# Optimization experiments

Hardware: AMD Instinct MI355X
Metric: run time of the kernel (lower is better)

The kernel has to match this reference:

```python
import jax, jax.numpy as jnp
import numpy as np


def _conv1x1(x, w):
    # x [N,I,D,H,W], w [O,I]
    return jnp.einsum('nidhw,oi->nodhw', x, w)


def _conv3x3(x, w):
    return jax.lax.conv_general_dilated(
        x, w, window_strides=(1, 1, 1), padding=[(1, 1)] * 3,
        dimension_numbers=('NCDHW', 'OIDHW', 'NCDHW'))


def _interp_axis(x, out_len, axis):
    # linear interpolation along one axis, align_corners=True
    in_len = x.shape[axis]
    scale = (in_len - 1) / (out_len - 1)
    pos = jnp.arange(out_len, dtype=x.dtype) * scale
    lo = jnp.clip(jnp.floor(pos).astype(jnp.int32), 0, in_len - 1)
    hi = jnp.minimum(lo + 1, in_len - 1)
    frac = pos - lo.astype(x.dtype)
    shp = [1] * x.ndim
    shp[axis] = out_len
    frac = frac.reshape(shp)
    return jnp.take(x, lo, axis=axis) * (1 - frac) + jnp.take(x, hi, axis=axis) * frac


def _upsample_trilinear_ac(x, size):
    for ax, s in zip((2, 3, 4), size):
        x = _interp_axis(x, s, ax)
    return x


def _grid_sample_3d(inp, grid):
    # inp [N,C,D,H,W]; grid [N,Do,Ho,Wo,3] with channels (x=w, y=h, z=d) in [-1,1]
    # matches torch grid_sample defaults: trilinear, align_corners=False, zeros padding
    N, C, D, H, W = inp.shape
    ix = ((grid[..., 0] + 1) * W - 1) * 0.5
    iy = ((grid[..., 1] + 1) * H - 1) * 0.5
    iz = ((grid[..., 2] + 1) * D - 1) * 0.5
    x0 = jnp.floor(ix).astype(jnp.int32)
    y0 = jnp.floor(iy).astype(jnp.int32)
    z0 = jnp.floor(iz).astype(jnp.int32)
    fx = ix - x0.astype(inp.dtype)
    fy = iy - y0.astype(inp.dtype)
    fz = iz - z0.astype(inp.dtype)
    flat = inp.reshape(N, C, D * H * W)
    out = jnp.zeros((N, C) + grid.shape[1:4], dtype=inp.dtype)
    for dz, wz in ((0, 1 - fz), (1, fz)):
        for dy, wy in ((0, 1 - fy), (1, fy)):
            for dx, wx in ((0, 1 - fx), (1, fx)):
                zc = z0 + dz
                yc = y0 + dy
                xc = x0 + dx
                valid = (zc >= 0) & (zc < D) & (yc >= 0) & (yc < H) & (xc >= 0) & (xc < W)
                idx = (jnp.clip(zc, 0, D - 1) * H + jnp.clip(yc, 0, H - 1)) * W + jnp.clip(xc, 0, W - 1)
                vals = jax.vmap(lambda f, i: f[:, i])(flat, idx)  # [N,C,Do,Ho,Wo]
                w = (wz * wy * wx) * valid.astype(inp.dtype)
                out = out + vals * w[:, None]
    return out


def _point_reinforce(x, w_atten, w_conv):
    # SE-style: global avg pool -> 1x1 conv -> sigmoid -> residual scale -> 1x1 conv
    pooled = jnp.mean(x, axis=(2, 3, 4), keepdims=True)
    atten = jax.nn.sigmoid(_conv1x1(pooled, w_atten))
    x = x + x * atten
    return _conv1x1(x, w_conv)


def _forward(x, y, w_down_h, w_down_l, w_flow, w_att_atten, w_att_conv):
    D, H, W = x.shape[2:]
    low = _conv1x1(x, w_down_l)
    low = _point_reinforce(low, w_att_atten, w_att_conv)
    hf = _conv1x1(y, w_down_h)
    hf = _upsample_trilinear_ac(hf, (D, H, W))
    flow = _conv3x3(jnp.concatenate([hf, low], axis=1), w_flow)  # [N,3,D,H,W]
    # coordinate grid, channel order (w, h, d) as in the original flow_warp
    gw = jnp.broadcast_to(jnp.arange(W, dtype=x.dtype)[None, None, :], (D, H, W))
    gh = jnp.broadcast_to(jnp.arange(H, dtype=x.dtype)[None, :, None], (D, H, W))
    gd = jnp.broadcast_to(jnp.arange(D, dtype=x.dtype)[:, None, None], (D, H, W))
    grid = jnp.stack([gw, gh, gd], axis=0)[None]  # [1,3,D,H,W]
    norm = jnp.array([W, H, D], dtype=x.dtype)
    # NOTE: faithful to original -- divides by size only (grid ends up in [0,1), not [-1,1])
    vgrid = jnp.transpose(grid + flow, (0, 2, 3, 4, 1)) / norm  # [N,D,H,W,3]
    return _grid_sample_3d(y, vgrid)


def setup_inputs() -> dict:
    key = jax.random.key(0)
    ks = jax.random.split(key, 7)
    inplane_l, inplane_h, outplane = 64, 128, 64
    x = jax.random.normal(ks[0], (2, inplane_l, 16, 64, 64), dtype=jnp.float32)
    y = jax.random.normal(ks[1], (2, inplane_h, 8, 32, 32), dtype=jnp.float32)
    s = 0.05
    w_down_h = jax.random.normal(ks[2], (outplane, inplane_h), dtype=jnp.float32) * s
    w_down_l = jax.random.normal(ks[3], (outplane, inplane_l), dtype=jnp.float32) * s
    w_flow = jax.random.normal(ks[4], (3, 2 * outplane, 3, 3, 3), dtype=jnp.float32) * s
    w_att_atten = jax.random.normal(ks[5], (inplane_l, inplane_l), dtype=jnp.float32) * s
    w_att_conv = jax.random.normal(ks[6], (inplane_l, inplane_l), dtype=jnp.float32) * s
    return {'x': x, 'y': y, 'w_down_h': w_down_h, 'w_down_l': w_down_l,
            'w_flow': w_flow, 'w_att_atten': w_att_atten, 'w_att_conv': w_att_conv}


def reference(x, y, w_down_h, w_down_l, w_flow, w_att_atten, w_att_conv):
    return _forward(x, y, w_down_h, w_down_l, w_flow, w_att_atten, w_att_conv)
```

## Files before the change

kernel.cpp:

```cpp
#include <hip/hip_runtime.h>
#include <math.h>


#define MEANX_OFF  0
#define WCOMBT_OFF 128
#define HF_OFF     8320
#define LOW2_OFF   1056896
#define HFUP_OFF   9445504
#define VG_OFF     17834112
#define ZPAGE_OFF  18227328

__global__ __launch_bounds__(256) void kearly(const float* __restrict__ x,
                                              const float* __restrict__ y,
                                              const float* __restrict__ wdh,
                                              float* __restrict__ meanx,
                                              float* __restrict__ hf,
                                              float* __restrict__ zpage) {
    const int blk = blockIdx.x;
    if (blk < 128) {
        if (blk == 0 && threadIdx.x < 64) zpage[threadIdx.x] = 0.f;
        int ch = blk;
        const float4* base = (const float4*)(x + (size_t)ch * 65536);
        float s = 0.f;
        for (int j = threadIdx.x; j < 16384; j += 256) {
            float4 v = base[j];
            s += v.x + v.y + v.z + v.w;
        }
        __shared__ float red[256];
        red[threadIdx.x] = s;
        __syncthreads();
        for (int off = 128; off > 0; off >>= 1) {
            if (threadIdx.x < off) red[threadIdx.x] += red[threadIdx.x + off];
            __syncthreads();
        }
        if (threadIdx.x == 0) meanx[ch] = red[0] * (1.0f / 65536.0f);
    } else {
        const int b = blk - 128;
        const int n = b >> 7;
        const int r = b & 127;
        const int os = r & 3;
        const int tile = r >> 2;
        const int p = tile * 256 + threadIdx.x;
        const float* yb = y + (size_t)n * 128 * 8192 + p;

        float acc[16];
#pragma unroll
        for (int o = 0; o < 16; ++o) acc[o] = 0.f;

        for (int i = 0; i < 128; i += 4) {
            const float yi0 = yb[(size_t)(i + 0) * 8192];
            const float yi1 = yb[(size_t)(i + 1) * 8192];
            const float yi2 = yb[(size_t)(i + 2) * 8192];
            const float yi3 = yb[(size_t)(i + 3) * 8192];
#pragma unroll
            for (int o = 0; o < 16; ++o) {
                float a = acc[o];
                a = fmaf(wdh[(os * 16 + o) * 128 + i + 0], yi0, a);
                a = fmaf(wdh[(os * 16 + o) * 128 + i + 1], yi1, a);
                a = fmaf(wdh[(os * 16 + o) * 128 + i + 2], yi2, a);
                a = fmaf(wdh[(os * 16 + o) * 128 + i + 3], yi3, a);
                acc[o] = a;
            }
        }
        float* ob = hf + (size_t)(n * 64 + os * 16) * 8192 + p;
#pragma unroll
        for (int o = 0; o < 16; ++o)
            ob[(size_t)o * 8192] = acc[o];
    }
}

__global__ __launch_bounds__(256) void kprep(const float* __restrict__ wdl,
                                             const float* __restrict__ watt,
                                             const float* __restrict__ wconv,
                                             const float* __restrict__ meanx,
                                             float* __restrict__ wcombT) {
    const int n = blockIdx.x;
    const int tid = threadIdx.x;
    __shared__ float s_wdl[4096];
    __shared__ float s_wcT[4096];
    __shared__ float pooled[64], sc[64];
    for (int k = tid; k < 4096; k += 256) {
        s_wdl[k] = wdl[k];
        int o = k >> 6, j = k & 63;
        s_wcT[j * 64 + o] = wconv[k];
    }
    __syncthreads();
    if (tid < 64) {
        float p = 0.f;
        for (int i = 0; i < 64; ++i) p += s_wdl[tid * 64 + i] * meanx[n * 64 + i];
        pooled[tid] = p;
    }
    __syncthreads();
    if (tid < 64) {
        float a = 0.f;
        for (int i = 0; i < 64; ++i) a += watt[tid * 64 + i] * pooled[i];
        sc[tid] = 1.f + 1.f / (1.f + expf(-a));
    }
    __syncthreads();
    for (int k = 0; k < 16; ++k) {
        const int idx = tid + 256 * k;
        const int o = idx & 63, i = idx >> 6;
        float acc = 0.f;
#pragma unroll 8
        for (int j = 0; j < 64; ++j)
            acc += s_wcT[j * 64 + o] * (sc[j] * s_wdl[j * 64 + i]);
        wcombT[n * 4096 + i * 64 + o] = acc;
    }
}

__global__ __launch_bounds__(256) void kmid(const float* __restrict__ x,
                                            const float* __restrict__ wcombT,
                                            const float* __restrict__ hf,
                                            float* __restrict__ low2,
                                            float* __restrict__ hfup) {
    const int blk = blockIdx.x;
    if (blk < 512) {
        const int b = blk;
        const int n = b >> 8;
        const int r = b & 255;
        const int os = r & 1;
        const int tile = r >> 1;
        const int p = tile * 512 + 2 * threadIdx.x;
        const float* xb = x + (size_t)n * 64 * 65536 + p;
        const float* wr = wcombT + n * 4096 + os * 32;

        float2 acc[32];
#pragma unroll
        for (int o = 0; o < 32; ++o) acc[o] = make_float2(0.f, 0.f);

        for (int i = 0; i < 64; i += 2) {
            const float2 xi0 = *(const float2*)(xb + (size_t)(i + 0) * 65536);
            const float2 xi1 = *(const float2*)(xb + (size_t)(i + 1) * 65536);
#pragma unroll
            for (int o = 0; o < 32; ++o) {
                const float w0 = wr[(i + 0) * 64 + o];
                const float w1 = wr[(i + 1) * 64 + o];
                acc[o].x = fmaf(w0, xi0.x, acc[o].x);
                acc[o].y = fmaf(w0, xi0.y, acc[o].y);
                acc[o].x = fmaf(w1, xi1.x, acc[o].x);
                acc[o].y = fmaf(w1, xi1.y, acc[o].y);
            }
        }
        float* ob = low2 + (size_t)(n * 64 + os * 32) * 65536 + p;
#pragma unroll
        for (int o = 0; o < 32; ++o)
            *(float2*)(ob + (size_t)o * 65536) = acc[o];
    } else {
        int id2 = (blk - 512) * 256 + threadIdx.x;
        int wp = id2 & 31, h = (id2 >> 5) & 63, d = (id2 >> 11) & 15;
        int c = (id2 >> 15) & 63, n = id2 >> 21;
        const float SD = 7.0f / 15.0f, SH = 31.0f / 63.0f;
        float pd = (float)d * SD, ph = (float)h * SH;
        int z0 = (int)pd; if (z0 > 7) z0 = 7;
        int z1 = min(z0 + 1, 7); float fz = pd - (float)z0;
        int y0 = (int)ph; if (y0 > 31) y0 = 31;
        int y1 = min(y0 + 1, 31); float fy = ph - (float)y0;

        const int w0i = 2 * wp, w1i = 2 * wp + 1;
        float pw0 = (float)w0i * SH, pw1 = (float)w1i * SH;
        int xa = (int)pw0; if (xa > 31) xa = 31;
        float fx0 = pw0 - (float)xa;
        int xb2 = (int)pw1; if (xb2 > 31) xb2 = 31;
        float fx1 = pw1 - (float)xb2;

        const float* b = hf + (size_t)(n * 64 + c) * 8192;
        const int r00 = (z0 * 32 + y0) * 32, r01 = (z0 * 32 + y1) * 32;
        const int r10 = (z1 * 32 + y0) * 32, r11 = (z1 * 32 + y1) * 32;
        const float wzy00 = (1.f - fz) * (1.f - fy), wzy01 = (1.f - fz) * fy;
        const float wzy10 = fz * (1.f - fy), wzy11 = fz * fy;

        float colv[3];
#pragma unroll
        for (int j = 0; j < 3; ++j) {
            int xc = min(xa + j, 31);
            colv[j] = wzy00 * b[r00 + xc] + wzy01 * b[r01 + xc] +
                      wzy10 * b[r10 + xc] + wzy11 * b[r11 + xc];
        }
        float o0 = colv[0] + (colv[1] - colv[0]) * fx0;
        int i1 = xb2 - xa;
        float lo = (i1 == 0) ? colv[0] : colv[1];
        float hi = (i1 == 0) ? colv[1] : colv[2];
        float o1 = lo + (hi - lo) * fx1;

        *(float2*)(hfup + ((size_t)id2 * 2)) = make_float2(o0, o1);
    }
}

__global__ __launch_bounds__(256) void kflowp(const float* __restrict__ ws,
                                              const float* __restrict__ wflow,
                                              float* __restrict__ part) {
    const int tid = threadIdx.x;
    const int b = blockIdx.x;
    const int split = b & 15;
    const int tile = b >> 4;
    const int n = tile >> 6;
    const int t = tile & 63;
    const int td = t >> 4, th = (t >> 2) & 3, tw = t & 3;
    const int d0 = td * 4, h0 = th * 16, w0 = tw * 16;
    const int xo = tid & 3, ty = (tid >> 2) & 15, tz = tid >> 6;
    const int wv = tid >> 6;

    __shared__ float lds[3][2048];

    const int srcb = (split < 8)
        ? HFUP_OFF + (n * 64 + split * 8) * 65536
        : LOW2_OFF + (n * 64 + (split - 8) * 8) * 65536;

    int woff[8];
#pragma unroll
    for (int k = 0; k < 8; ++k) {
        const int e = tid + 256 * k;
        const int r = e / 18;
        const int lx = e - r * 18;
        const int z = r / 18;
        const int ly = r - z * 18;
        const int gz = d0 - 1 + z, gy = h0 - 1 + ly, gx = w0 - 1 + lx;
        const bool ok = (e < 1944) && ((unsigned)gz < 16u) && ((unsigned)gy < 64u) &&
                        ((unsigned)gx < 64u);
        woff[k] = ok ? (srcb + gz * 4096 + gy * 64 + gx) : ZPAGE_OFF;
    }

#define STAGE(BUFI, CI)                                                               \
    {                                                                                 \
        _Pragma("unroll")                                                             \
        for (int k = 0; k < 8; ++k) {                                                 \
            const int off = woff[k] + ((woff[k] < ZPAGE_OFF) ? (CI) * 65536 : 0);     \
            __builtin_amdgcn_global_load_lds(                                         \
                (const __attribute__((address_space(1))) unsigned int*)(ws + off),    \
                (__attribute__((address_space(3))) unsigned int*)                     \
                    (&lds[BUFI][wv * 64 + 256 * k]),                                  \
                4, 0, 0);                                                             \
        }                                                                             \
    }

    float acc[3][4];
#pragma unroll
    for (int o = 0; o < 3; ++o)
#pragma unroll
        for (int j = 0; j < 4; ++j) acc[o][j] = 0.f;

    STAGE(0, 0);

    for (int ci = 0; ci < 8; ++ci) {
        const int cur = ci % 3;
        if (ci < 7) {
            STAGE((ci + 1) % 3, ci + 1);
            asm volatile("s_waitcnt vmcnt(8)" ::: "memory");
        } else {
            asm volatile("s_waitcnt vmcnt(0)" ::: "memory");
        }
        __builtin_amdgcn_s_barrier();
        __builtin_amdgcn_sched_barrier(0);

        const int cgs = __builtin_amdgcn_readfirstlane(split * 8 + ci);
        const float* wb = wflow + (size_t)cgs * 27;
        const float* buf = lds[cur];
        __builtin_amdgcn_s_setprio(1);
#pragma unroll
        for (int dz = 0; dz < 3; ++dz) {
#pragma unroll
            for (int dy = 0; dy < 3; ++dy) {
                const float* rp = &buf[((tz + dz) * 18 + ty + dy) * 18 + 4 * xo];
                const float2 a0 = *(const float2*)(rp);
                const float2 a1 = *(const float2*)(rp + 2);
                const float2 a2 = *(const float2*)(rp + 4);
                const float v[6] = {a0.x, a0.y, a1.x, a1.y, a2.x, a2.y};
                float wq[3][3];
#pragma unroll
                for (int o = 0; o < 3; ++o)
#pragma unroll
                    for (int dx = 0; dx < 3; ++dx)
                        wq[o][dx] = wb[o * 3456 + (dz * 3 + dy) * 3 + dx];
#pragma unroll
                for (int o = 0; o < 3; ++o)
#pragma unroll
                    for (int j = 0; j < 4; ++j)
#pragma unroll
                        for (int dx = 0; dx < 3; ++dx)
                            acc[o][j] = fmaf(wq[o][dx], v[j + dx], acc[o][j]);
            }
        }
        __builtin_amdgcn_s_setprio(0);
    }
#undef STAGE

    const int oz = d0 + tz, oy = h0 + ty, ox = w0 + 4 * xo;
    const size_t base = ((size_t)(split * 2 + n)) * 3 * 65536;
    const int p = oz * 4096 + oy * 64 + ox;
#pragma unroll
    for (int o = 0; o < 3; ++o)
        *(float4*)(part + base + (size_t)o * 65536 + p) =
            make_float4(acc[o][0], acc[o][1], acc[o][2], acc[o][3]);
}

__global__ __launch_bounds__(256) void kpost(const float* __restrict__ part,
                                             const float* __restrict__ y,
                                             float* __restrict__ vg,
                                             float* __restrict__ yt) {
    const int blk = blockIdx.x;
    if (blk < 512) {
        int gid = blk * 256 + threadIdx.x;
        int n = gid >> 16, p = gid & 65535;
        float s0 = 0.f, s1 = 0.f, s2 = 0.f;
        for (int s = 0; s < 16; ++s) {
            const float* bp = part + ((size_t)(s * 2 + n)) * 3 * 65536 + p;
            s0 += bp[0];
            s1 += bp[65536];
            s2 += bp[131072];
        }
        int w = p & 63, h = (p >> 6) & 63, d = p >> 12;
        size_t vb = (size_t)n * 3 * 65536;
        vg[vb + p]          = ((float)w + s0) * (1.0f / 64.0f);
        vg[vb + 65536 + p]  = ((float)h + s1) * (1.0f / 64.0f);
        vg[vb + 131072 + p] = ((float)d + s2) * (1.0f / 16.0f);
    } else {
        int b = blk - 512;
        int n = b >> 8;
        int rem = b & 255;
        int ct = rem >> 7, st = rem & 127;
        int c0 = ct * 64, s0 = st * 64;
        __shared__ float t[64][65];
        int tx = threadIdx.x & 63, ty = threadIdx.x >> 6;
#pragma unroll
        for (int k = 0; k < 16; ++k)
            t[ty + 4 * k][tx] = y[((size_t)(n * 128 + c0 + ty + 4 * k)) * 8192 + s0 + tx];
        __syncthreads();
#pragma unroll
        for (int k = 0; k < 16; ++k)
            yt[((size_t)(n * 8192 + s0 + ty + 4 * k)) * 128 + c0 + tx] = t[tx][ty + 4 * k];
    }
}

__global__ __launch_bounds__(256) void ksample(const float* __restrict__ yt,
                                               const float* __restrict__ vg,
                                               float* __restrict__ out) {
    const int b = blockIdx.x;
    const int n = b >> 10;
    const int p0 = (b & 1023) << 6;
    const int tid = threadIdx.x;
    const int lane = tid & 63;
    const int wv = tid >> 6;

    __shared__ float lds[128 * 65];

    const float* ytn = yt + (size_t)n * 8192 * 128;
    const size_t vb = (size_t)n * 3 * 65536;

    for (int q = 0; q < 16; ++q) {
        const int pt = wv * 16 + q;
        const int p = p0 + pt;
        float gx = vg[vb + p], gy = vg[vb + 65536 + p], gz = vg[vb + 131072 + p];
        float ix = ((gx + 1.f) * 32.f - 1.f) * 0.5f;
        float iy = ((gy + 1.f) * 32.f - 1.f) * 0.5f;
        float iz = ((gz + 1.f) * 8.f - 1.f) * 0.5f;
        int x0 = (int)floorf(ix), y0 = (int)floorf(iy), z0 = (int)floorf(iz);
        float fx = ix - (float)x0, fy = iy - (float)y0, fz = iz - (float)z0;
        float wx[2] = {1.f - fx, fx}, wy[2] = {1.f - fy, fy}, wz[2] = {1.f - fz, fz};
        int idx8[8];
        float w8[8];
        float wsum = 0.f;
#pragma unroll
        for (int k = 0; k < 8; ++k) {
            int dz = k >> 2, dy = (k >> 1) & 1, dx = k & 1;
            int zc = z0 + dz, yc = y0 + dy, xc = x0 + dx;
            bool valid = ((unsigned)zc < 8u) && ((unsigned)yc < 32u) && ((unsigned)xc < 32u);
            int zcl = min(max(zc, 0), 7), ycl = min(max(yc, 0), 31), xcl = min(max(xc, 0), 31);
            idx8[k] = (zcl * 32 + ycl) * 32 + xcl;
            float wgt = wz[dz] * wy[dy] * wx[dx];
            w8[k] = valid ? wgt : 0.f;
            wsum += w8[k];
        }
        float ax = 0.f, ay = 0.f;
        if (wsum != 0.f) {
#pragma unroll
            for (int k = 0; k < 8; ++k) {
                const float2 v = *(const float2*)(ytn + (size_t)idx8[k] * 128 + 2 * lane);
                ax = fmaf(w8[k], v.x, ax);
                ay = fmaf(w8[k], v.y, ay);
            }
        }
        lds[(2 * lane) * 65 + pt] = ax;
        lds[(2 * lane + 1) * 65 + pt] = ay;
    }
    __syncthreads();
    const int pw = tid & 63, cw = tid >> 6;
    float* ob = out + (size_t)n * 128 * 65536 + p0 + pw;
#pragma unroll
    for (int k = 0; k < 32; ++k) {
        int c = k * 4 + cw;
        ob[(size_t)c * 65536] = lds[c * 65 + pw];
    }
}

extern "C" void kernel_launch(void* const* d_in, const int* in_sizes, int n_in,
                              void* d_out, int out_size, void* d_ws, size_t ws_size,
                              hipStream_t stream) {
    const float* x     = (const float*)d_in[0];
    const float* y     = (const float*)d_in[1];
    const float* wdh   = (const float*)d_in[2];
    const float* wdl   = (const float*)d_in[3];
    const float* wflow = (const float*)d_in[4];
    const float* watt  = (const float*)d_in[5];
    const float* wconv = (const float*)d_in[6];
    float* out = (float*)d_out;

    float* ws     = (float*)d_ws;
    float* meanx  = ws + MEANX_OFF;
    float* wcombT = ws + WCOMBT_OFF;
    float* hf     = ws + HF_OFF;
    float* low2   = ws + LOW2_OFF;
    float* hfup   = ws + HFUP_OFF;
    float* vg     = ws + VG_OFF;
    float* zpage  = ws + ZPAGE_OFF;

    float* part = out;
    float* yt = hfup;

    kearly<<<384, 256, 0, stream>>>(x, y, wdh, meanx, hf, zpage);
    kprep<<<2, 256, 0, stream>>>(wdl, watt, wconv, meanx, wcombT);
    kmid<<<16896, 256, 0, stream>>>(x, wcombT, hf, low2, hfup);
    kflowp<<<2048, 256, 0, stream>>>(ws, wflow, part);
    kpost<<<1024, 256, 0, stream>>>(part, y, vg, yt);
    ksample<<<2048, 256, 0, stream>>>(yt, vg, out);
}
```

Measured before the change: 173.1 us.

## Reduce flow conv split-K partials with atomics and fold grid normalize into sampler

Instead of writing 16 split partial flow fields and summing them in a separate pass, the flow kernel now atomically adds its results into one zero-initialised buffer, which extra blocks appended to the mid kernel clear. The grid offset and normalisation move into the sampling kernel, so the post kernel only does the transpose of y. The idea is to avoid writing and re-reading about 6 MB of partials, at the cost of float atomics with contention (16-way per element) and a nondeterministic summation order. The s_setprio hints in the conv loop are also removed.

New measurement: 223.1 us. 28.9% more time.

```diff
diff --git a/kernel.cpp b/kernel.cpp
--- a/kernel.cpp
+++ b/kernel.cpp
@@ -112,7 +112,8 @@
                                             const float* __restrict__ wcombT,
                                             const float* __restrict__ hf,
                                             float* __restrict__ low2,
-                                            float* __restrict__ hfup) {
+                                            float* __restrict__ hfup,
+                                            float* __restrict__ vgsum) {
     const int blk = blockIdx.x;
     if (blk < 512) {
         const int b = blk;
@@ -145,7 +146,7 @@
 #pragma unroll
         for (int o = 0; o < 32; ++o)
             *(float2*)(ob + (size_t)o * 65536) = acc[o];
-    } else {
+    } else if (blk < 16896) {
         int id2 = (blk - 512) * 256 + threadIdx.x;
         int wp = id2 & 31, h = (id2 >> 5) & 63, d = (id2 >> 11) & 15;
         int c = (id2 >> 15) & 63, n = id2 >> 21;
@@ -183,12 +184,17 @@
         float o1 = lo + (hi - lo) * fx1;
 
         *(float2*)(hfup + ((size_t)id2 * 2)) = make_float2(o0, o1);
+    } else {
+        const int idx = (blk - 16896) * 256 + threadIdx.x;
+        float4 z4 = make_float4(0.f, 0.f, 0.f, 0.f);
+        *(float4*)(vgsum + (size_t)idx * 8) = z4;
+        *(float4*)(vgsum + (size_t)idx * 8 + 4) = z4;
     }
 }
 
 __global__ __launch_bounds__(256) void kflowp(const float* __restrict__ ws,
                                               const float* __restrict__ wflow,
-                                              float* __restrict__ part) {
+                                              float* __restrict__ vgsum) {
     const int tid = threadIdx.x;
     const int b = blockIdx.x;
     const int split = b & 15;
@@ -255,7 +261,6 @@
         const int cgs = __builtin_amdgcn_readfirstlane(split * 8 + ci);
         const float* wb = wflow + (size_t)cgs * 27;
         const float* buf = lds[cur];
-        __builtin_amdgcn_s_setprio(1);
 #pragma unroll
         for (int dz = 0; dz < 3; ++dz) {
 #pragma unroll
@@ -280,59 +285,39 @@
                             acc[o][j] = fmaf(wq[o][dx], v[j + dx], acc[o][j]);
             }
         }
-        __builtin_amdgcn_s_setprio(0);
     }
 #undef STAGE
 
     const int oz = d0 + tz, oy = h0 + ty, ox = w0 + 4 * xo;
-    const size_t base = ((size_t)(split * 2 + n)) * 3 * 65536;
     const int p = oz * 4096 + oy * 64 + ox;
+    float* vs = vgsum + (size_t)n * 3 * 65536;
 #pragma unroll
     for (int o = 0; o < 3; ++o)
-        *(float4*)(part + base + (size_t)o * 65536 + p) =
-            make_float4(acc[o][0], acc[o][1], acc[o][2], acc[o][3]);
-}
-
-__global__ __launch_bounds__(256) void kpost(const float* __restrict__ part,
-                                             const float* __restrict__ y,
-                                             float* __restrict__ vg,
+#pragma unroll
+        for (int j = 0; j < 4; ++j)
+            unsafeAtomicAdd(vs + (size_t)o * 65536 + p + j, acc[o][j]);
+}
+
+__global__ __launch_bounds__(256) void kpost(const float* __restrict__ y,
                                              float* __restrict__ yt) {
-    const int blk = blockIdx.x;
-    if (blk < 512) {
-        int gid = blk * 256 + threadIdx.x;
-        int n = gid >> 16, p = gid & 65535;
-        float s0 = 0.f, s1 = 0.f, s2 = 0.f;
-        for (int s = 0; s < 16; ++s) {
-            const float* bp = part + ((size_t)(s * 2 + n)) * 3 * 65536 + p;
-            s0 += bp[0];
-            s1 += bp[65536];
-            s2 += bp[131072];
-        }
-        int w = p & 63, h = (p >> 6) & 63, d = p >> 12;
-        size_t vb = (size_t)n * 3 * 65536;
-        vg[vb + p]          = ((float)w + s0) * (1.0f / 64.0f);
-        vg[vb + 65536 + p]  = ((float)h + s1) * (1.0f / 64.0f);
-        vg[vb + 131072 + p] = ((float)d + s2) * (1.0f / 16.0f);
-    } else {
-        int b = blk - 512;
-        int n = b >> 8;
-        int rem = b & 255;
-        int ct = rem >> 7, st = rem & 127;
-        int c0 = ct * 64, s0 = st * 64;
-        __shared__ float t[64][65];
-        int tx = threadIdx.x & 63, ty = threadIdx.x >> 6;
-#pragma unroll
-        for (int k = 0; k < 16; ++k)
-            t[ty + 4 * k][tx] = y[((size_t)(n * 128 + c0 + ty + 4 * k)) * 8192 + s0 + tx];
-        __syncthreads();
-#pragma unroll
-        for (int k = 0; k < 16; ++k)
-            yt[((size_t)(n * 8192 + s0 + ty + 4 * k)) * 128 + c0 + tx] = t[tx][ty + 4 * k];
-    }
+    int b = blockIdx.x;
+    int n = b >> 8;
+    int rem = b & 255;
+    int ct = rem >> 7, st = rem & 127;
+    int c0 = ct * 64, s0 = st * 64;
+    __shared__ float t[64][65];
+    int tx = threadIdx.x & 63, ty = threadIdx.x >> 6;
+#pragma unroll
+    for (int k = 0; k < 16; ++k)
+        t[ty + 4 * k][tx] = y[((size_t)(n * 128 + c0 + ty + 4 * k)) * 8192 + s0 + tx];
+    __syncthreads();
+#pragma unroll
+    for (int k = 0; k < 16; ++k)
+        yt[((size_t)(n * 8192 + s0 + ty + 4 * k)) * 128 + c0 + tx] = t[tx][ty + 4 * k];
 }
 
 __global__ __launch_bounds__(256) void ksample(const float* __restrict__ yt,
-                                               const float* __restrict__ vg,
+                                               const float* __restrict__ vgsum,
                                                float* __restrict__ out) {
     const int b = blockIdx.x;
     const int n = b >> 10;
@@ -349,7 +334,11 @@
     for (int q = 0; q < 16; ++q) {
         const int pt = wv * 16 + q;
         const int p = p0 + pt;
-        float gx = vg[vb + p], gy = vg[vb + 65536 + p], gz = vg[vb + 131072 + p];
+        const int w = p & 63, h = (p >> 6) & 63, d = p >> 12;
+        float s0 = vgsum[vb + p], s1 = vgsum[vb + 65536 + p], s2 = vgsum[vb + 131072 + p];
+        float gx = ((float)w + s0) * (1.0f / 64.0f);
+        float gy = ((float)h + s1) * (1.0f / 64.0f);
+        float gz = ((float)d + s2) * (1.0f / 16.0f);
         float ix = ((gx + 1.f) * 32.f - 1.f) * 0.5f;
         float iy = ((gy + 1.f) * 32.f - 1.f) * 0.5f;
         float iz = ((gz + 1.f) * 8.f - 1.f) * 0.5f;
@@ -410,16 +399,15 @@
     float* hf     = ws + HF_OFF;
     float* low2   = ws + LOW2_OFF;
     float* hfup   = ws + HFUP_OFF;
-    float* vg     = ws + VG_OFF;
+    float* vgsum  = ws + VG_OFF;
     float* zpage  = ws + ZPAGE_OFF;
 
-    float* part = out;
     float* yt = hfup;
 
     kearly<<<384, 256, 0, stream>>>(x, y, wdh, meanx, hf, zpage);
     kprep<<<2, 256, 0, stream>>>(wdl, watt, wconv, meanx, wcombT);
-    kmid<<<16896, 256, 0, stream>>>(x, wcombT, hf, low2, hfup);
-    kflowp<<<2048, 256, 0, stream>>>(ws, wflow, part);
-    kpost<<<1024, 256, 0, stream>>>(part, y, vg, yt);
-    ksample<<<2048, 256, 0, stream>>>(yt, vg, out);
-}
+    kmid<<<17088, 256, 0, stream>>>(x, wcombT, hf, low2, hfup, vgsum);
+    kflowp<<<2048, 256, 0, stream>>>(ws, wflow, vgsum);
+    kpost<<<512, 256, 0, stream>>>(y, yt);
+    ksample<<<2048, 256, 0, stream>>>(yt, vgsum, out);
+}
```
